# Performance work log

Measured on AMD Instinct MI355X. Metric: run time of the kernel, lower is better.

Reference implementation:

```python
import jax, jax.numpy as jnp
import numpy as np

D = 1024
H = 16
HD = D // H

def setup_inputs() -> dict:
    key = jax.random.key(0)
    ks = jax.random.split(key, 6)
    tokens = jax.random.normal(ks[0], (2, 2048, D), dtype=jnp.float32)
    # LayerNorm params
    ln_gamma = jnp.ones((D,), dtype=jnp.float32)
    ln_beta = jnp.zeros((D,), dtype=jnp.float32)
    # qkv Linear (no bias): torch Linear weight is [3D, D]; store as [D, 3D] for x @ W
    w_qkv = jax.random.normal(ks[1], (D, 3 * D), dtype=jnp.float32) / np.sqrt(D)
    # output projection with bias
    w_proj = jax.random.normal(ks[2], (D, D), dtype=jnp.float32) / np.sqrt(D)
    b_proj = jax.random.normal(ks[3], (D,), dtype=jnp.float32) * 0.01
    return {"tokens": tokens, "ln_gamma": ln_gamma, "ln_beta": ln_beta,
            "w_qkv": w_qkv, "w_proj": w_proj, "b_proj": b_proj}

def reference(tokens, ln_gamma, ln_beta, w_qkv, w_proj, b_proj):
    B, S, _ = tokens.shape
    res = tokens
    # LayerNorm (eps=1e-5, torch default)
    mu = jnp.mean(tokens, axis=-1, keepdims=True)
    var = jnp.var(tokens, axis=-1, keepdims=True)
    x = (tokens - mu) * jax.lax.rsqrt(var + 1e-5) * ln_gamma + ln_beta
    # QKV projection -> [B, S, 3, H, HD] -> q,k,v each [B, H, S, HD]
    qkv = (x @ w_qkv).reshape(B, S, 3, H, HD)
    qkv = jnp.transpose(qkv, (2, 0, 3, 1, 4))
    q, k, v = qkv[0], qkv[1], qkv[2]
    scale = HD ** -0.5
    scores = jnp.einsum('bhsd,bhtd->bhst', q, k) * scale  # [B,H,S,S]
    attn = jax.nn.softmax(scores, axis=-1)
    dots = jnp.einsum('bhst,bhtd->bhsd', attn, v)          # [B,H,S,HD]
    dots = jnp.transpose(dots, (0, 2, 1, 3)).reshape(B, S, D)
    out = dots @ w_proj + b_proj
    return out + res
```

## Files before the change

### kernel.cpp

```cpp
#include <hip/hip_runtime.h>

typedef __bf16 bf16x8 __attribute__((ext_vector_type(8)));
typedef __bf16 bf16x4 __attribute__((ext_vector_type(4)));
typedef float f32x4 __attribute__((ext_vector_type(4)));
typedef unsigned short us8 __attribute__((ext_vector_type(8)));

__device__ __forceinline__ unsigned short f2bf(float f) {
  unsigned int u = __builtin_bit_cast(unsigned int, f);
  u += 0x7FFFu + ((u >> 16) & 1u);
  return (unsigned short)(u >> 16);
}
__device__ __forceinline__ float bf2f(unsigned short s) {
  return __builtin_bit_cast(float, (unsigned int)s << 16);
}

__device__ __forceinline__ void load_lds16(const void* g, void* l) {
  __builtin_amdgcn_global_load_lds(
      (const __attribute__((address_space(1))) unsigned int*)g,
      (__attribute__((address_space(3))) unsigned int*)l, 16, 0, 0);
}

#define MFMA16(a, b, c) __builtin_amdgcn_mfma_f32_16x16x32_bf16(a, b, c, 0, 0, 0)

constexpr int Dm = 1024, Ss = 2048;

__global__ __launch_bounds__(256) void ln_kernel(
    const float* __restrict__ x, const float* __restrict__ gamma,
    const float* __restrict__ beta, unsigned short* __restrict__ out) {
  const int row = blockIdx.x;
  const int t = threadIdx.x;
  const float4 v = reinterpret_cast<const float4*>(x + (size_t)row * Dm)[t];
  float s = v.x + v.y + v.z + v.w;
  float ss = v.x * v.x + v.y * v.y + v.z * v.z + v.w * v.w;
#pragma unroll
  for (int off = 1; off < 64; off <<= 1) {
    s += __shfl_xor(s, off);
    ss += __shfl_xor(ss, off);
  }
  __shared__ float sb[8];
  const int lane = t & 63, wid = t >> 6;
  if (lane == 0) { sb[wid] = s; sb[4 + wid] = ss; }
  __syncthreads();
  s = sb[0] + sb[1] + sb[2] + sb[3];
  ss = sb[4] + sb[5] + sb[6] + sb[7];
  const float mu = s * (1.0f / Dm);
  const float var = ss * (1.0f / Dm) - mu * mu;
  const float rs = rsqrtf(var + 1e-5f);
  const float4 g = reinterpret_cast<const float4*>(gamma)[t];
  const float4 bt = reinterpret_cast<const float4*>(beta)[t];
  ushort4 pack;
  pack.x = f2bf((v.x - mu) * rs * g.x + bt.x);
  pack.y = f2bf((v.y - mu) * rs * g.y + bt.y);
  pack.z = f2bf((v.z - mu) * rs * g.z + bt.z);
  pack.w = f2bf((v.w - mu) * rs * g.w + bt.w);
  reinterpret_cast<ushort4*>(out + (size_t)row * Dm)[t] = pack;
}

__global__ __launch_bounds__(256) void transpose_kernel(
    const float* __restrict__ in, unsigned short* __restrict__ out, int K, int N) {
  __shared__ float tile[32][33];
  const int tx = threadIdx.x & 31, ty = threadIdx.x >> 5;
  const int n0 = blockIdx.x * 32, k0 = blockIdx.y * 32;
#pragma unroll
  for (int i = 0; i < 4; i++)
    tile[ty + i * 8][tx] = in[(size_t)(k0 + ty + i * 8) * N + n0 + tx];
  __syncthreads();
#pragma unroll
  for (int i = 0; i < 4; i++)
    out[(size_t)(n0 + ty + i * 8) * K + k0 + tx] = f2bf(tile[tx][ty + i * 8]);
}

template <int EPI, int BN>
__global__ __launch_bounds__(256) void gemm_kernel(
    const unsigned short* __restrict__ A, const unsigned short* __restrict__ Bt,
    int N, int K, int nbx, unsigned short* __restrict__ Cbf,
    unsigned short* __restrict__ vt, float* __restrict__ Cf,
    const float* __restrict__ bias, const float* __restrict__ resid) {
  __shared__ unsigned short Al[128 * 64];
  __shared__ unsigned short Bl[BN * 64];
  constexpr int NJ = BN / 32;
  const int tid = threadIdx.x;
  const int lane = tid & 63, wid = tid >> 6;
  const int l15 = lane & 15, lg = lane >> 4;
  const int wm = wid >> 1, wn = wid & 1;
  const int cpx = gridDim.x >> 3;
  const int lb = (blockIdx.x & 7) * cpx + (blockIdx.x >> 3);
  const int bx = lb % nbx, by = lb / nbx;
  const int bm = by * 128, bn = bx * BN;
  const int r8 = lane >> 3;
  const int swz = ((lane & 7) * 16) ^ (r8 << 4);
  const char* Ab = (const char*)A;
  const char* Bb = (const char*)Bt;
  f32x4 acc[4][NJ] = {};
  for (int k0 = 0; k0 < K; k0 += 64) {
    __syncthreads();
#pragma unroll
    for (int p = 0; p < 4; p++) {
      const int row = p * 32 + wid * 8 + r8;
      load_lds16(Ab + ((size_t)(bm + row) * K + k0) * 2 + swz,
                 (char*)Al + p * 4096 + wid * 1024);
    }
#pragma unroll
    for (int p = 0; p < BN / 32; p++) {
      const int row = p * 32 + wid * 8 + r8;
      load_lds16(Bb + ((size_t)(bn + row) * K + k0) * 2 + swz,
                 (char*)Bl + p * 4096 + wid * 1024);
    }
    __syncthreads();
#pragma unroll
    for (int kk = 0; kk < 2; kk++) {
      bf16x8 af[4], bfr[NJ];
#pragma unroll
      for (int mi = 0; mi < 4; mi++) {
        const int row = wm * 64 + mi * 16 + l15;
        af[mi] = *(const bf16x8*)((const char*)Al + row * 128 +
                                  ((kk * 64 + lg * 16) ^ ((row & 7) << 4)));
      }
#pragma unroll
      for (int nj = 0; nj < NJ; nj++) {
        const int row = wn * (BN / 2) + nj * 16 + l15;
        bfr[nj] = *(const bf16x8*)((const char*)Bl + row * 128 +
                                   ((kk * 64 + lg * 16) ^ ((row & 7) << 4)));
      }
#pragma unroll
      for (int mi = 0; mi < 4; mi++)
#pragma unroll
        for (int nj = 0; nj < NJ; nj++)
          acc[mi][nj] = MFMA16(af[mi], bfr[nj], acc[mi][nj]);
    }
  }
#pragma unroll
  for (int mi = 0; mi < 4; mi++)
#pragma unroll
    for (int nj = 0; nj < NJ; nj++) {
      const int m = bm + wm * 64 + mi * 16 + lg * 4;
      const int n = bn + wn * (BN / 2) + nj * 16 + l15;
      if (EPI == 0) {
        if (n < 2048) {
          const float sc = (n < 1024) ? 0.180336880f : 1.0f;
#pragma unroll
          for (int r = 0; r < 4; r++)
            Cbf[(size_t)(m + r) * N + n] = f2bf(acc[mi][nj][r] * sc);
        } else {
          const int h = (n - 2048) >> 6, hd = (n - 2048) & 63;
          const int bq = m >> 11, s = m & 2047;
          bf16x4 o;
#pragma unroll
          for (int r = 0; r < 4; r++) o[r] = (__bf16)acc[mi][nj][r];
          *(bf16x4*)(vt + ((size_t)((bq << 4) + h) * 64 + hd) * 2048 + s) = o;
        }
      } else {
#pragma unroll
        for (int r = 0; r < 4; r++) {
          const size_t idx = (size_t)(m + r) * N + n;
          Cf[idx] = acc[mi][nj][r] + bias[n] + resid[idx];
        }
      }
    }
}

__global__ __launch_bounds__(512) void attn_kernel(
    const unsigned short* __restrict__ qkv, const unsigned short* __restrict__ vt,
    unsigned short* part0, unsigned short* part1, float* __restrict__ ml) {
  __shared__ unsigned short Kb[2][64 * 64];
  __shared__ unsigned short Vb[2][64 * 64];
  __shared__ unsigned short Pl[8][32][64];
  const int tid = threadIdx.x, lane = tid & 63, wid = tid >> 6;
  const int l15 = lane & 15, lg = lane >> 4;
  const int lb = (blockIdx.x & 7) * 64 + (blockIdx.x >> 3);
  const int bh = lb >> 4, qt = (lb >> 1) & 7, half = lb & 1;
  const int b = bh >> 4, h = bh & 15;
  const int q0 = qt * 256 + wid * 32;
  const unsigned short* qbase = qkv + (size_t)(b * Ss) * 3072 + h * 64;
  const char* kbase = (const char*)(qkv + (size_t)(b * Ss) * 3072 + 1024 + h * 64);
  const char* vbase = (const char*)(vt + (size_t)bh * 64 * Ss);

  bf16x8 qf[2][2];
#pragma unroll
  for (int qj = 0; qj < 2; qj++)
#pragma unroll
    for (int kk = 0; kk < 2; kk++)
      qf[qj][kk] = *reinterpret_cast<const bf16x8*>(
          &qbase[(size_t)(q0 + qj * 16 + l15) * 3072 + kk * 32 + lg * 8]);

  f32x4 accT[4][2] = {};
  float psum[2] = {0.f, 0.f};

  const int srow = lane >> 3;
  const int swz = ((lane & 7) * 16) ^ (srow << 4);

#define STAGE(bufi, t0v)                                                          \
  {                                                                               \
    load_lds16(kbase + (size_t)((t0v) + wid * 8 + srow) * 6144 + swz,             \
               (char*)&Kb[bufi][0] + wid * 1024);                                 \
    load_lds16(vbase + (size_t)(wid * 8 + srow) * 4096 + (size_t)(t0v) * 2 + swz, \
               (char*)&Vb[bufi][0] + wid * 1024);                                 \
  }

  const int t0base = half * 1024;
  STAGE(0, t0base);

  for (int itr = 0; itr < 16; itr++) {
    const int cur = itr & 1;
    asm volatile("s_waitcnt vmcnt(0)" ::: "memory");
    __builtin_amdgcn_s_barrier();
    if (itr + 1 < 16) STAGE(cur ^ 1, t0base + (itr + 1) * 64);

    const char* kcur = (const char*)&Kb[cur][0];
    const char* vcur = (const char*)&Vb[cur][0];

    f32x4 accs[4][2] = {};
    __builtin_amdgcn_s_setprio(1);
#pragma unroll
    for (int kk = 0; kk < 2; kk++) {
      bf16x8 kf[4];
#pragma unroll
      for (int kvi = 0; kvi < 4; kvi++) {
        const int rk = kvi * 16 + l15;
        kf[kvi] = *(const bf16x8*)(kcur + rk * 128 +
                                   ((kk * 64 + lg * 16) ^ ((rk & 7) << 4)));
      }
#pragma unroll
      for (int kvi = 0; kvi < 4; kvi++)
#pragma unroll
        for (int qj = 0; qj < 2; qj++)
          accs[kvi][qj] = MFMA16(kf[kvi], qf[qj][kk], accs[kvi][qj]);
    }
    __builtin_amdgcn_s_setprio(0);

#pragma unroll
    for (int qj = 0; qj < 2; qj++) {
      const int prow = qj * 16 + l15;
      char* prl = (char*)&Pl[wid][prow][0];
      float ps = 0.f;
#pragma unroll
      for (int kvi = 0; kvi < 4; kvi++) {
        bf16x4 pk;
#pragma unroll
        for (int r = 0; r < 4; r++) {
          const float p = exp2f(accs[kvi][qj][r]);
          ps += p;
          pk[r] = (__bf16)p;
        }
        *(bf16x4*)(prl + ((kvi * 32 + lg * 8) ^ ((l15 & 7) << 4))) = pk;
      }
      psum[qj] += ps;
    }

    asm volatile("s_waitcnt lgkmcnt(0)" ::: "memory");
    __builtin_amdgcn_sched_barrier(0);

    __builtin_amdgcn_s_setprio(1);
#pragma unroll
    for (int kk2 = 0; kk2 < 2; kk2++) {
      bf16x8 pf[2], vf[4];
#pragma unroll
      for (int qj = 0; qj < 2; qj++)
        pf[qj] = *(const bf16x8*)((const char*)&Pl[wid][qj * 16 + l15][0] +
                                  ((kk2 * 64 + lg * 16) ^ ((l15 & 7) << 4)));
#pragma unroll
      for (int nj = 0; nj < 4; nj++) {
        const int rv = nj * 16 + l15;
        vf[nj] = *(const bf16x8*)(vcur + rv * 128 +
                                  ((kk2 * 64 + lg * 16) ^ ((rv & 7) << 4)));
      }
#pragma unroll
      for (int nj = 0; nj < 4; nj++)
#pragma unroll
        for (int qj = 0; qj < 2; qj++)
          accT[nj][qj] = MFMA16(vf[nj], pf[qj], accT[nj][qj]);
    }
    __builtin_amdgcn_s_setprio(0);
  }

#pragma unroll
  for (int qj = 0; qj < 2; qj++) {
    psum[qj] += __shfl_xor(psum[qj], 16);
    psum[qj] += __shfl_xor(psum[qj], 32);
  }
  unsigned short* pout = half ? part1 : part0;
#pragma unroll
  for (int qj = 0; qj < 2; qj++) {
    const float rl = 1.0f / psum[qj];
    const int q = q0 + qj * 16 + l15;
#pragma unroll
    for (int nj = 0; nj < 4; nj++) {
      bf16x4 o;
#pragma unroll
      for (int r = 0; r < 4; r++) o[r] = (__bf16)(accT[nj][qj][r] * rl);
      *(bf16x4*)(pout + (size_t)(b * Ss + q) * Dm + h * 64 + nj * 16 + lg * 4) = o;
    }
  }
  if (lg == 0) {
#pragma unroll
    for (int qj = 0; qj < 2; qj++)
      ml[half * 65536 + bh * 2048 + q0 + qj * 16 + l15] = __log2f(psum[qj]);
  }
}

__global__ __launch_bounds__(256) void combine_kernel(
    const unsigned short* p0, const unsigned short* __restrict__ p1,
    const float* __restrict__ ml, unsigned short* dots) {
  const int t = blockIdx.x * 256 + threadIdx.x;
  const int hd8 = t & 7;
  const int h = (t >> 3) & 15;
  const int row = t >> 7;
  const int b = row >> 11, s = row & 2047;
  const int bh = b * 16 + h;
  const float s0 = ml[bh * 2048 + s];
  const float s1 = ml[65536 + bh * 2048 + s];
  const float M = fmaxf(s0, s1);
  float w0 = exp2f(s0 - M), w1 = exp2f(s1 - M);
  const float inv = 1.0f / (w0 + w1);
  w0 *= inv; w1 *= inv;
  const size_t off = (size_t)row * 1024 + h * 64 + hd8 * 8;
  const us8 a = *(const us8*)(p0 + off);
  const us8 c = *(const us8*)(p1 + off);
  us8 o;
#pragma unroll
  for (int j = 0; j < 8; j++) o[j] = f2bf(w0 * bf2f(a[j]) + w1 * bf2f(c[j]));
  *(us8*)(dots + off) = o;
}

extern "C" void kernel_launch(void* const* d_in, const int* in_sizes, int n_in,
                              void* d_out, int out_size, void* d_ws, size_t ws_size,
                              hipStream_t stream) {
  const float* tokens = (const float*)d_in[0];
  const float* ln_g = (const float*)d_in[1];
  const float* ln_b = (const float*)d_in[2];
  const float* w_qkv = (const float*)d_in[3];
  const float* w_proj = (const float*)d_in[4];
  const float* b_proj = (const float*)d_in[5];
  float* out = (float*)d_out;

  char* ws = (char*)d_ws;
  unsigned short* x_bf = (unsigned short*)(ws);
  unsigned short* wqkvT = (unsigned short*)(ws + 8388608);
  unsigned short* wprojT = (unsigned short*)(ws + 14680064);
  unsigned short* qkvraw = (unsigned short*)(ws + 16777216);
  unsigned short* vt = (unsigned short*)(ws + 41943040);
  unsigned short* part1 = (unsigned short*)(ws + 50331648);
  float* ml = (float*)(ws + 58720256);
  unsigned short* dots = x_bf;

  ln_kernel<<<4096, 256, 0, stream>>>(tokens, ln_g, ln_b, x_bf);
  transpose_kernel<<<dim3(3072 / 32, 1024 / 32), 256, 0, stream>>>(w_qkv, wqkvT, 1024, 3072);
  transpose_kernel<<<dim3(1024 / 32, 1024 / 32), 256, 0, stream>>>(w_proj, wprojT, 1024, 1024);
  gemm_kernel<0, 128><<<768, 256, 0, stream>>>(
      x_bf, wqkvT, 3072, 1024, 24, qkvraw, vt, nullptr, nullptr, nullptr);
  attn_kernel<<<512, 512, 0, stream>>>(qkvraw, vt, dots, part1, ml);
  combine_kernel<<<2048, 256, 0, stream>>>(dots, part1, ml, dots);
  gemm_kernel<1, 64><<<512, 256, 0, stream>>>(
      dots, wprojT, 1024, 1024, 16, nullptr, nullptr, out, b_proj, tokens);
}
```

Measured before the change: 137.4 us.

## Split attention KV range four ways and shrink P staging buffer

The attention kernel becomes templated on a KV split factor. When the workspace is large enough it launches 1024 blocks, each covering a quarter of the keys, and combine_kernel merges four partial outputs. The P tile in LDS is halved by writing and consuming it in two 32-column chunks, and the launch bounds now request higher occupancy. The aim is more blocks to fill the GPU and less LDS per block. The cost is extra partial-output traffic, a heavier combine pass, and more LDS waits and sync points per iteration.

Result: slower. 337.0 us (+145.3%).

```diff
diff --git a/kernel.cpp b/kernel.cpp
--- a/kernel.cpp
+++ b/kernel.cpp
@@ -159,16 +159,21 @@
     }
 }
 
-__global__ __launch_bounds__(512) void attn_kernel(
+template <int LOGSP>
+__global__ __launch_bounds__(512, 6) void attn_kernel(
     const unsigned short* __restrict__ qkv, const unsigned short* __restrict__ vt,
-    unsigned short* part0, unsigned short* part1, float* __restrict__ ml) {
+    unsigned short* p0, unsigned short* p1, unsigned short* p2, unsigned short* p3,
+    float* __restrict__ ml) {
   __shared__ unsigned short Kb[2][64 * 64];
   __shared__ unsigned short Vb[2][64 * 64];
-  __shared__ unsigned short Pl[8][32][64];
+  __shared__ unsigned short Pl[8][32][32];
   const int tid = threadIdx.x, lane = tid & 63, wid = tid >> 6;
   const int l15 = lane & 15, lg = lane >> 4;
-  const int lb = (blockIdx.x & 7) * 64 + (blockIdx.x >> 3);
-  const int bh = lb >> 4, qt = (lb >> 1) & 7, half = lb & 1;
+  const int cpx = gridDim.x >> 3;
+  const int lb = (blockIdx.x & 7) * cpx + (blockIdx.x >> 3);
+  const int sp = lb & ((1 << LOGSP) - 1);
+  const int qt = (lb >> LOGSP) & 7;
+  const int bh = lb >> (3 + LOGSP);
   const int b = bh >> 4, h = bh & 15;
   const int q0 = qt * 256 + wid * 32;
   const unsigned short* qbase = qkv + (size_t)(b * Ss) * 3072 + h * 64;
@@ -197,14 +202,15 @@
                (char*)&Vb[bufi][0] + wid * 1024);                                 \
   }
 
-  const int t0base = half * 1024;
+  const int t0base = sp * (2048 >> LOGSP);
+  const int NIT = 32 >> LOGSP;
   STAGE(0, t0base);
 
-  for (int itr = 0; itr < 16; itr++) {
+  for (int itr = 0; itr < NIT; itr++) {
     const int cur = itr & 1;
     asm volatile("s_waitcnt vmcnt(0)" ::: "memory");
     __builtin_amdgcn_s_barrier();
-    if (itr + 1 < 16) STAGE(cur ^ 1, t0base + (itr + 1) * 64);
+    if (itr + 1 < NIT) STAGE(cur ^ 1, t0base + (itr + 1) * 64);
 
     const char* kcur = (const char*)&Kb[cur][0];
     const char* vcur = (const char*)&Vb[cur][0];
@@ -228,6 +234,7 @@
     }
     __builtin_amdgcn_s_setprio(0);
 
+    bf16x4 pk1[2][2];
 #pragma unroll
     for (int qj = 0; qj < 2; qj++) {
       const int prow = qj * 16 + l15;
@@ -235,14 +242,17 @@
       float ps = 0.f;
 #pragma unroll
       for (int kvi = 0; kvi < 4; kvi++) {
-        bf16x4 pk;
+        bf16x4 pkv;
 #pragma unroll
         for (int r = 0; r < 4; r++) {
           const float p = exp2f(accs[kvi][qj][r]);
           ps += p;
-          pk[r] = (__bf16)p;
+          pkv[r] = (__bf16)p;
         }
-        *(bf16x4*)(prl + ((kvi * 32 + lg * 8) ^ ((l15 & 7) << 4))) = pk;
+        if (kvi < 2)
+          *(bf16x4*)(prl + (((kvi & 1) * 32 + lg * 8) ^ ((l15 & 3) << 4))) = pkv;
+        else
+          pk1[qj][kvi - 2] = pkv;
       }
       psum[qj] += ps;
     }
@@ -250,27 +260,59 @@
     asm volatile("s_waitcnt lgkmcnt(0)" ::: "memory");
     __builtin_amdgcn_sched_barrier(0);
 
-    __builtin_amdgcn_s_setprio(1);
-#pragma unroll
-    for (int kk2 = 0; kk2 < 2; kk2++) {
+    {
       bf16x8 pf[2], vf[4];
 #pragma unroll
       for (int qj = 0; qj < 2; qj++)
         pf[qj] = *(const bf16x8*)((const char*)&Pl[wid][qj * 16 + l15][0] +
-                                  ((kk2 * 64 + lg * 16) ^ ((l15 & 7) << 4)));
+                                  ((lg * 16) ^ ((l15 & 3) << 4)));
 #pragma unroll
       for (int nj = 0; nj < 4; nj++) {
         const int rv = nj * 16 + l15;
         vf[nj] = *(const bf16x8*)(vcur + rv * 128 +
-                                  ((kk2 * 64 + lg * 16) ^ ((rv & 7) << 4)));
-      }
+                                  ((lg * 16) ^ ((rv & 7) << 4)));
+      }
+      asm volatile("s_waitcnt lgkmcnt(0)" ::: "memory");
+      __builtin_amdgcn_sched_barrier(0);
+      __builtin_amdgcn_s_setprio(1);
 #pragma unroll
       for (int nj = 0; nj < 4; nj++)
 #pragma unroll
         for (int qj = 0; qj < 2; qj++)
           accT[nj][qj] = MFMA16(vf[nj], pf[qj], accT[nj][qj]);
-    }
-    __builtin_amdgcn_s_setprio(0);
+      __builtin_amdgcn_s_setprio(0);
+#pragma unroll
+      for (int qj = 0; qj < 2; qj++) {
+        char* prl = (char*)&Pl[wid][qj * 16 + l15][0];
+#pragma unroll
+        for (int k2 = 0; k2 < 2; k2++)
+          *(bf16x4*)(prl + ((k2 * 32 + lg * 8) ^ ((l15 & 3) << 4))) = pk1[qj][k2];
+      }
+    }
+
+    asm volatile("s_waitcnt lgkmcnt(0)" ::: "memory");
+    __builtin_amdgcn_sched_barrier(0);
+
+    {
+      bf16x8 pf[2], vf[4];
+#pragma unroll
+      for (int qj = 0; qj < 2; qj++)
+        pf[qj] = *(const bf16x8*)((const char*)&Pl[wid][qj * 16 + l15][0] +
+                                  ((lg * 16) ^ ((l15 & 3) << 4)));
+#pragma unroll
+      for (int nj = 0; nj < 4; nj++) {
+        const int rv = nj * 16 + l15;
+        vf[nj] = *(const bf16x8*)(vcur + rv * 128 +
+                                  ((64 + lg * 16) ^ ((rv & 7) << 4)));
+      }
+      __builtin_amdgcn_s_setprio(1);
+#pragma unroll
+      for (int nj = 0; nj < 4; nj++)
+#pragma unroll
+        for (int qj = 0; qj < 2; qj++)
+          accT[nj][qj] = MFMA16(vf[nj], pf[qj], accT[nj][qj]);
+      __builtin_amdgcn_s_setprio(0);
+    }
   }
 
 #pragma unroll
@@ -278,7 +320,7 @@
     psum[qj] += __shfl_xor(psum[qj], 16);
     psum[qj] += __shfl_xor(psum[qj], 32);
   }
-  unsigned short* pout = half ? part1 : part0;
+  unsigned short* pout = (sp == 0) ? p0 : (sp == 1) ? p1 : (sp == 2) ? p2 : p3;
 #pragma unroll
   for (int qj = 0; qj < 2; qj++) {
     const float rl = 1.0f / psum[qj];
@@ -294,12 +336,14 @@
   if (lg == 0) {
 #pragma unroll
     for (int qj = 0; qj < 2; qj++)
-      ml[half * 65536 + bh * 2048 + q0 + qj * 16 + l15] = __log2f(psum[qj]);
-  }
-}
-
+      ml[sp * 65536 + bh * 2048 + q0 + qj * 16 + l15] = psum[qj];
+  }
+}
+
+template <int NS>
 __global__ __launch_bounds__(256) void combine_kernel(
     const unsigned short* p0, const unsigned short* __restrict__ p1,
+    const unsigned short* __restrict__ p2, const unsigned short* __restrict__ p3,
     const float* __restrict__ ml, unsigned short* dots) {
   const int t = blockIdx.x * 256 + threadIdx.x;
   const int hd8 = t & 7;
@@ -307,18 +351,25 @@
   const int row = t >> 7;
   const int b = row >> 11, s = row & 2047;
   const int bh = b * 16 + h;
-  const float s0 = ml[bh * 2048 + s];
-  const float s1 = ml[65536 + bh * 2048 + s];
-  const float M = fmaxf(s0, s1);
-  float w0 = exp2f(s0 - M), w1 = exp2f(s1 - M);
-  const float inv = 1.0f / (w0 + w1);
-  w0 *= inv; w1 *= inv;
+  float w[NS], tot = 0.f;
+#pragma unroll
+  for (int i = 0; i < NS; i++) {
+    w[i] = ml[i * 65536 + bh * 2048 + s];
+    tot += w[i];
+  }
+  const float inv = 1.0f / tot;
   const size_t off = (size_t)row * 1024 + h * 64 + hd8 * 8;
-  const us8 a = *(const us8*)(p0 + off);
-  const us8 c = *(const us8*)(p1 + off);
+  const unsigned short* ps[4] = {p0, p1, p2, p3};
+  float acc[8] = {};
+#pragma unroll
+  for (int i = 0; i < NS; i++) {
+    const us8 a = *(const us8*)(ps[i] + off);
+#pragma unroll
+    for (int j = 0; j < 8; j++) acc[j] += bf2f(a[j]) * w[i];
+  }
   us8 o;
 #pragma unroll
-  for (int j = 0; j < 8; j++) o[j] = f2bf(w0 * bf2f(a[j]) + w1 * bf2f(c[j]));
+  for (int j = 0; j < 8; j++) o[j] = f2bf(acc[j] * inv);
   *(us8*)(dots + off) = o;
 }
 
@@ -340,7 +391,9 @@
   unsigned short* qkvraw = (unsigned short*)(ws + 16777216);
   unsigned short* vt = (unsigned short*)(ws + 41943040);
   unsigned short* part1 = (unsigned short*)(ws + 50331648);
-  float* ml = (float*)(ws + 58720256);
+  unsigned short* part2 = (unsigned short*)(ws + 58720256);
+  unsigned short* part3 = (unsigned short*)(ws + 67108864);
+  float* ml = (float*)(ws + 75497472);
   unsigned short* dots = x_bf;
 
   ln_kernel<<<4096, 256, 0, stream>>>(tokens, ln_g, ln_b, x_bf);
@@ -348,8 +401,13 @@
   transpose_kernel<<<dim3(1024 / 32, 1024 / 32), 256, 0, stream>>>(w_proj, wprojT, 1024, 1024);
   gemm_kernel<0, 128><<<768, 256, 0, stream>>>(
       x_bf, wqkvT, 3072, 1024, 24, qkvraw, vt, nullptr, nullptr, nullptr);
-  attn_kernel<<<512, 512, 0, stream>>>(qkvraw, vt, dots, part1, ml);
-  combine_kernel<<<2048, 256, 0, stream>>>(dots, part1, ml, dots);
+  if (ws_size >= 76600000ull) {
+    attn_kernel<2><<<1024, 512, 0, stream>>>(qkvraw, vt, dots, part1, part2, part3, ml);
+    combine_kernel<4><<<2048, 256, 0, stream>>>(dots, part1, part2, part3, ml, dots);
+  } else {
+    attn_kernel<1><<<512, 512, 0, stream>>>(qkvraw, vt, dots, part1, part1, part1, ml);
+    combine_kernel<2><<<2048, 256, 0, stream>>>(dots, part1, part1, part1, ml, dots);
+  }
   gemm_kernel<1, 64><<<512, 256, 0, stream>>>(
       dots, wprojT, 1024, 1024, 16, nullptr, nullptr, out, b_proj, tokens);
 }
```
